# Performance work log

Measured on AMD Instinct MI355X. Metric: run time of the kernel, lower is better.

## Reference

```python
import jax, jax.numpy as jnp
import numpy as np
import math

D_MODEL = 512
N_HEADS = 8
PATH_LEN = 3
B, L, S = 4, 1024, 1024


def _path_index_structure(L, S, path_length):
    """Precompute the static multi-hop index structure (numpy, trace-time)."""
    i = np.arange(L)[:, None]          # [L,1]
    j = np.arange(S)[None, :]          # [1,S]
    step = (j - i) / path_length       # float
    # Python int() truncates toward zero; i + k*step >= 0 here, so floor == int().
    m1 = np.floor(i + 1 * step).astype(np.int32)  # [L,S] first intermediate point
    m2 = np.floor(i + 2 * step).astype(np.int32)  # [L,S] second intermediate point
    near = np.abs(i - j) <= path_length            # [L,S] bool: direct-score region
    return m1, m2, near


def setup_inputs() -> dict:
    key = jax.random.key(0)
    ks = jax.random.split(key, 7)
    inp = {
        "queries": jax.random.normal(ks[0], (B, L, D_MODEL), dtype=jnp.float32),
        "keys": jax.random.normal(ks[1], (B, S, D_MODEL), dtype=jnp.float32),
        "values": jax.random.normal(ks[2], (B, S, D_MODEL), dtype=jnp.float32),
        # nn.Linear(d_model, d_keys*n_heads, bias=False): stored as [in, out] so y = x @ W
        "W_q": jax.random.normal(ks[3], (D_MODEL, D_MODEL), dtype=jnp.float32) * 0.02,
        "W_k": jax.random.normal(ks[4], (D_MODEL, D_MODEL), dtype=jnp.float32) * 0.02,
        "W_v": jax.random.normal(ks[5], (D_MODEL, D_MODEL), dtype=jnp.float32) * 0.02,
        "W_o": jax.random.normal(ks[6], (D_MODEL, D_MODEL), dtype=jnp.float32) * 0.02,
    }
    return inp


def reference(queries, keys, values, W_q, W_k, W_v, W_o):
    Bv, Lv, _ = queries.shape
    Sv = keys.shape[1]
    H = N_HEADS
    q = (queries @ W_q).reshape(Bv, Lv, H, -1).transpose(0, 2, 1, 3)  # [B,H,L,D]
    k = (keys @ W_k).reshape(Bv, Sv, H, -1).transpose(0, 2, 1, 3)     # [B,H,S,D]
    v = (values @ W_v).reshape(Bv, Sv, H, -1).transpose(0, 2, 1, 3)   # [B,H,S,D]
    D = q.shape[-1]

    scores = jnp.einsum('bhld,bhsd->bhls', q, k) / math.sqrt(D)  # [B,H,L,S]

    # --- path-score modification (vectorized form of the nested loops) ---
    m1, m2, near = _path_index_structure(Lv, Sv, PATH_LEN)
    row = np.arange(Lv)[:, None]
    col = np.arange(Sv)[None, :]
    a = scores[:, :, row, m1]   # scores[:,:,i,m1(i,j)] -> [B,H,L,S]
    b = scores[:, :, m2, col]   # scores[:,:,m2(i,j),j] -> [B,H,L,S]
    # .mean() in the original reduces over BOTH batch and heads to a scalar per (i,j)
    path_mean = jnp.mean(a * b, axis=(0, 1))  # [L,S]
    scores = jnp.where(jnp.asarray(near), scores, path_mean[None, None, :, :])

    attn = jax.nn.softmax(scores, axis=-1)  # dropout p=0 in eval reference
    out = jnp.einsum('bhls,bhsd->blhd', attn, v).reshape(Bv, Lv, H * D)
    out = out @ W_o  # [B,L,d_model]
    return out, attn
```

## Files before the change

### kernel.cpp

```cpp
#include <hip/hip_runtime.h>
#include <math.h>

static constexpr int B_ = 4;
static constexpr int L_ = 1024;
static constexpr int S_ = 1024;
static constexpr int DMODEL = 512;
static constexpr int NH = 8;
static constexpr int DH = 64;
static constexpr int NBH = 32;

typedef __attribute__((ext_vector_type(8))) short s8;
typedef __attribute__((ext_vector_type(4))) float floatx4;

__device__ __forceinline__ short f2bf(float f) {
  unsigned u = __float_as_uint(f);
  return (short)((u + 0x7fffu + ((u >> 16) & 1u)) >> 16);
}
__device__ __forceinline__ float bf2f(short s) {
  return __uint_as_float(((unsigned)(unsigned short)s) << 16);
}

__global__ __launch_bounds__(256)
void prep_kernel(const float* __restrict__ q, const float* __restrict__ k,
                 const float* __restrict__ v, short* __restrict__ dst,
                 float* __restrict__ bandS,
                 const float* __restrict__ Wq, const float* __restrict__ Wk,
                 const float* __restrict__ Wv, const float* __restrict__ Wo,
                 short* __restrict__ WT) {
  __shared__ float t[32][33];
  if (blockIdx.x < 3072) {
    const int i = blockIdx.x * 256 + threadIdx.x;
    if (i < 32768) {
      const float4 m4 = make_float4(-1e30f, -1e30f, -1e30f, -1e30f);
      *(float4*)(bandS + ((size_t)i << 3)) = m4;
      *(float4*)(bandS + ((size_t)i << 3) + 4) = m4;
    }
    const int arr = i >> 18;
    const int off = (i & 262143) << 3;
    const float* src = (arr == 0) ? q : (arr == 1) ? k : v;
    const float4 f0 = *(const float4*)(src + off);
    const float4 f1 = *(const float4*)(src + off + 4);
    s8 o;
    o[0] = f2bf(f0.x); o[1] = f2bf(f0.y); o[2] = f2bf(f0.z); o[3] = f2bf(f0.w);
    o[4] = f2bf(f1.x); o[5] = f2bf(f1.y); o[6] = f2bf(f1.z); o[7] = f2bf(f1.w);
    *(s8*)(dst + (size_t)arr * 2097152 + off) = o;
  } else {
    const int bid2 = blockIdx.x - 3072;
    const int z = bid2 >> 8;
    const int rem = bid2 & 255;
    const int k0 = (rem >> 4) << 5, n0 = (rem & 15) << 5;
    const float* W = (z == 0) ? Wq : (z == 1) ? Wk : (z == 2) ? Wv : Wo;
    short* dw = WT + (size_t)z * 262144;
    const int row = threadIdx.x >> 3;
    const int c4 = (threadIdx.x & 7) << 2;
    const float4 f = *(const float4*)(W + (size_t)(k0 + row) * 512 + n0 + c4);
    t[row][c4 + 0] = f.x; t[row][c4 + 1] = f.y; t[row][c4 + 2] = f.z; t[row][c4 + 3] = f.w;
    __syncthreads();
#pragma unroll
    for (int j = 0; j < 4; ++j)
      dw[(size_t)(n0 + row) * 512 + k0 + c4 + j] = f2bf(t[c4 + j][row]);
  }
}

__global__ __launch_bounds__(256)
void proj_qkv_kernel(const short* __restrict__ xbf, const short* __restrict__ WTall,
                     short* __restrict__ qk, short* __restrict__ vT,
                     short* __restrict__ vS) {
  __shared__ short tileS[64][72];
  const int z = blockIdx.z;
  const short* A = xbf + (size_t)z * 2097152;
  const short* WT = WTall + (size_t)z * 262144;
  const int K = DMODEL;
  const int tid = threadIdx.x;
  const int lane = tid & 63, w = tid >> 6;
  const int wm = w >> 1, wn = w & 1;
  const int m0 = blockIdx.y * 64, n0 = blockIdx.x * 64;
  const int kl = (lane >> 4) << 3;
  const short* pA = A + (size_t)(m0 + wm * 32 + (lane & 15)) * K + kl;
  const short* pB = WT + (size_t)(n0 + wn * 32 + (lane & 15)) * K + kl;
  const size_t f16K = (size_t)16 * K;
  floatx4 acc00 = {0,0,0,0}, acc01 = {0,0,0,0}, acc10 = {0,0,0,0}, acc11 = {0,0,0,0};
  for (int k = 0; k < K; k += 32) {
    const s8 a0 = *(const s8*)(pA + k);
    const s8 a1 = *(const s8*)(pA + f16K + k);
    const s8 b0 = *(const s8*)(pB + k);
    const s8 b1 = *(const s8*)(pB + f16K + k);
    acc00 = __builtin_amdgcn_mfma_f32_16x16x32_bf16(a0, b0, acc00, 0, 0, 0);
    acc01 = __builtin_amdgcn_mfma_f32_16x16x32_bf16(a0, b1, acc01, 0, 0, 0);
    acc10 = __builtin_amdgcn_mfma_f32_16x16x32_bf16(a1, b0, acc10, 0, 0, 0);
    acc11 = __builtin_amdgcn_mfma_f32_16x16x32_bf16(a1, b1, acc11, 0, 0, 0);
  }
  const int crow = (lane >> 4) << 2;
  const int ccol = lane & 15;
  if (z < 2) {
#pragma unroll
    for (int fm = 0; fm < 2; ++fm)
#pragma unroll
      for (int fn = 0; fn < 2; ++fn) {
        const floatx4 acc = (fm == 0) ? ((fn == 0) ? acc00 : acc01)
                                      : ((fn == 0) ? acc10 : acc11);
#pragma unroll
        for (int r = 0; r < 4; ++r)
          tileS[wm * 32 + fm * 16 + crow + r][wn * 32 + fn * 16 + ccol] = f2bf(acc[r]);
      }
    __syncthreads();
    const int b = m0 >> 10, l0 = m0 & 1023, h = n0 >> 6;
    short* base = qk + (size_t)z * 2097152 + ((size_t)((b * NH + h) * L_ + l0)) * DH;
#pragma unroll
    for (int qk2 = 0; qk2 < 2; ++qk2) {
      const int c = tid + qk2 * 256;
      const int row = c >> 3, off = (c & 7) << 3;
      *(s8*)(base + (size_t)row * DH + off) = *(const s8*)&tileS[row][off];
    }
  } else {
#pragma unroll
    for (int fm = 0; fm < 2; ++fm)
#pragma unroll
      for (int fn = 0; fn < 2; ++fn) {
        const floatx4 acc = (fm == 0) ? ((fn == 0) ? acc00 : acc01)
                                      : ((fn == 0) ? acc10 : acc11);
        const int col = n0 + wn * 32 + fn * 16 + ccol;
#pragma unroll
        for (int r = 0; r < 4; ++r) {
          const int row = m0 + wm * 32 + fm * 16 + crow + r;
          const int b = row >> 10, l = row & 1023, h = col >> 6, d = col & 63;
          const short val = f2bf(acc[r]);
          vT[((size_t)((b * NH + h) * DH + d)) * S_ + l] = val;
          vS[((size_t)((b * NH + h) * S_ + l)) * DH + d] = val;
        }
      }
  }
}

__global__ __launch_bounds__(256)
void scores_bf16_kernel(const short* __restrict__ qbf, const short* __restrict__ kbf,
                        short* __restrict__ Sbf, float* __restrict__ bandS) {
  __shared__ short tileS[64][72];
  const int tid = threadIdx.x;
  const int lane = tid & 63, w = tid >> 6;
  const int wm = w >> 1, wn = w & 1;
  const int m0 = blockIdx.y * 64, n0 = blockIdx.x * 64;
  const int bh = blockIdx.z;
  const int kl = (lane >> 4) << 3;
  const short* pA = qbf + (size_t)bh * L_ * DH + (size_t)(m0 + wm * 32 + (lane & 15)) * DH + kl;
  const short* pB = kbf + (size_t)bh * S_ * DH + (size_t)(n0 + wn * 32 + (lane & 15)) * DH + kl;
  floatx4 acc00 = {0,0,0,0}, acc01 = {0,0,0,0}, acc10 = {0,0,0,0}, acc11 = {0,0,0,0};
#pragma unroll
  for (int k = 0; k < DH; k += 32) {
    const s8 a0 = *(const s8*)(pA + k);
    const s8 a1 = *(const s8*)(pA + 16 * DH + k);
    const s8 b0 = *(const s8*)(pB + k);
    const s8 b1 = *(const s8*)(pB + 16 * DH + k);
    acc00 = __builtin_amdgcn_mfma_f32_16x16x32_bf16(a0, b0, acc00, 0, 0, 0);
    acc01 = __builtin_amdgcn_mfma_f32_16x16x32_bf16(a0, b1, acc01, 0, 0, 0);
    acc10 = __builtin_amdgcn_mfma_f32_16x16x32_bf16(a1, b0, acc10, 0, 0, 0);
    acc11 = __builtin_amdgcn_mfma_f32_16x16x32_bf16(a1, b1, acc11, 0, 0, 0);
  }
  const int crow = (lane >> 4) << 2;
  const int ccol = lane & 15;
#pragma unroll
  for (int fm = 0; fm < 2; ++fm)
#pragma unroll
    for (int fn = 0; fn < 2; ++fn) {
      const floatx4 acc = (fm == 0) ? ((fn == 0) ? acc00 : acc01)
                                    : ((fn == 0) ? acc10 : acc11);
      const int col = n0 + wn * 32 + fn * 16 + ccol;
#pragma unroll
      for (int r = 0; r < 4; ++r) {
        const int row = m0 + wm * 32 + fm * 16 + crow + r;
        const float sc = acc[r] * 0.125f;
        tileS[wm * 32 + fm * 16 + crow + r][wn * 32 + fn * 16 + ccol] = f2bf(sc);
        const int dd = col - row;
        if (dd >= -3 && dd <= 3)
          bandS[(((size_t)bh << 10) + row) * 8 + dd + 3] = sc;
      }
    }
  __syncthreads();
  short* Sp = Sbf + ((size_t)bh << 20) + (size_t)m0 * S_ + n0;
#pragma unroll
  for (int q2 = 0; q2 < 2; ++q2) {
    const int c = tid + q2 * 256;
    const int row = c >> 3, off = (c & 7) << 3;
    *(s8*)(Sp + (size_t)row * S_ + off) = *(const s8*)&tileS[row][off];
  }
}

__global__ __launch_bounds__(256)
void path_mean_kernel(const short* __restrict__ Sbf, float* __restrict__ pm) {
  __shared__ float As[32][44];
  __shared__ float Bs[32][36];
  const int orig = blockIdx.x;
  const int wgid = (orig & 7) * 128 + (orig >> 3);
  const int i0 = (wgid >> 5) << 5;
  const int j0 = (wgid & 31) << 5;
  const int c0 = (2 * i0 + j0) / 3;
  const int c0a = c0 & ~7;
  const int r0 = (i0 + 2 * j0) / 3;
  const int tid = threadIdx.x;
  const int ti = tid >> 3;
  const int tj = tid & 7;
  const int gi = i0 + ti;
  int aoff[4], boff[4];
#pragma unroll
  for (int b = 0; b < 4; ++b) {
    const int gj = j0 + 4 * tj + b;
    const int m1 = (2 * gi + gj) / 3;
    const int m2 = (gi + 2 * gj) / 3;
    aoff[b] = ti * 44 + (m1 - c0a);
    boff[b] = (m2 - r0) * 36 + (4 * tj + b);
  }
  const int uA = tid;
  const int uB2 = tid + 256;
  int arow = 0, ac = 0, brow = 0, bc = 0, brow2 = 0, bc2 = 0;
  bool isA = uA < 160;
  if (isA) { arow = uA / 5; ac = uA - arow * 5; }
  else { const int v = uA - 160; brow = v >> 2; bc = v & 3; }
  const bool hasU2 = tid < 32;
  { const int v = uB2 - 160; brow2 = v >> 2; bc2 = v & 3; }
  int gcA = c0a + (ac << 3); if (gcA > 1016) gcA = 1016;
  const short* pA = Sbf + (size_t)(i0 + arow) * S_ + gcA;
  const short* pB = Sbf + (size_t)(r0 + brow) * S_ + j0 + (bc << 3);
  const short* pB2 = Sbf + (size_t)(r0 + brow2) * S_ + j0 + (bc2 << 3);

  const float* As0 = &As[0][0];
  const float* Bs0 = &Bs[0][0];
  float acc[4] = {0.f, 0.f, 0.f, 0.f};
  for (int z = 0; z < NBH; ++z) {
    const size_t zo = (size_t)z << 20;
    const s8 v1 = isA ? *(const s8*)(pA + zo) : *(const s8*)(pB + zo);
    s8 v2;
    if (hasU2) v2 = *(const s8*)(pB2 + zo);
    __syncthreads();
    {
      float4 lo, hi;
      lo.x = bf2f(v1[0]); lo.y = bf2f(v1[1]); lo.z = bf2f(v1[2]); lo.w = bf2f(v1[3]);
      hi.x = bf2f(v1[4]); hi.y = bf2f(v1[5]); hi.z = bf2f(v1[6]); hi.w = bf2f(v1[7]);
      if (isA) {
        *(float4*)&As[arow][ac << 3] = lo;
        *(float4*)&As[arow][(ac << 3) + 4] = hi;
      } else {
        *(float4*)&Bs[brow][bc << 3] = lo;
        *(float4*)&Bs[brow][(bc << 3) + 4] = hi;
      }
      if (hasU2) {
        float4 lo2, hi2;
        lo2.x = bf2f(v2[0]); lo2.y = bf2f(v2[1]); lo2.z = bf2f(v2[2]); lo2.w = bf2f(v2[3]);
        hi2.x = bf2f(v2[4]); hi2.y = bf2f(v2[5]); hi2.z = bf2f(v2[6]); hi2.w = bf2f(v2[7]);
        *(float4*)&Bs[brow2][bc2 << 3] = lo2;
        *(float4*)&Bs[brow2][(bc2 << 3) + 4] = hi2;
      }
    }
    __syncthreads();
#pragma unroll
    for (int b = 0; b < 4; ++b)
      acc[b] = fmaf(As0[aoff[b]], Bs0[boff[b]], acc[b]);
  }
  float4 o = make_float4(acc[0] * (1.f / 32.f), acc[1] * (1.f / 32.f),
                         acc[2] * (1.f / 32.f), acc[3] * (1.f / 32.f));
  *(float4*)&pm[(size_t)gi * S_ + j0 + 4 * tj] = o;
}

__global__ __launch_bounds__(256)
void pm_stats_kernel(const float* __restrict__ pm, short* __restrict__ E,
                     float* __restrict__ pmmax, float* __restrict__ pmsum) {
  const int wid = threadIdx.x >> 6, lane = threadIdx.x & 63;
  const int i = blockIdx.x * 4 + wid;
  const float* row = pm + (size_t)i * S_;
  const int j0 = lane << 4;
  float v[16];
#pragma unroll
  for (int c = 0; c < 4; ++c) {
    const float4 f = *(const float4*)(row + j0 + c * 4);
    v[c * 4 + 0] = f.x; v[c * 4 + 1] = f.y; v[c * 4 + 2] = f.z; v[c * 4 + 3] = f.w;
  }
  float mx = -1e30f;
#pragma unroll
  for (int u = 0; u < 16; ++u) {
    const int d = i - (j0 + u);
    const bool far = (d > 3) || (d < -3);
    if (far) mx = fmaxf(mx, v[u]);
  }
#pragma unroll
  for (int off = 32; off >= 1; off >>= 1) mx = fmaxf(mx, __shfl_xor(mx, off));
  float sum = 0.f;
  short e[16];
#pragma unroll
  for (int u = 0; u < 16; ++u) {
    const int d = i - (j0 + u);
    const bool far = (d > 3) || (d < -3);
    const float ev = far ? __expf(v[u] - mx) : 0.f;
    sum += ev;
    e[u] = f2bf(ev);
  }
#pragma unroll
  for (int off = 32; off >= 1; off >>= 1) sum += __shfl_xor(sum, off);
  s8 o0, o1;
#pragma unroll
  for (int u = 0; u < 8; ++u) { o0[u] = e[u]; o1[u] = e[8 + u]; }
  short* Erow = E + (size_t)i * S_ + j0;
  *(s8*)Erow = o0;
  *(s8*)(Erow + 8) = o1;
  if (lane == 0) { pmmax[i] = mx; pmsum[i] = sum; }
}

__global__ __launch_bounds__(256)
void ev_fused_kernel(const short* __restrict__ E, const short* __restrict__ vT,
                     const short* __restrict__ vS, const float* __restrict__ bandS,
                     const float* __restrict__ pmmax, const float* __restrict__ pmsum,
                     float* __restrict__ attn, short* __restrict__ out1) {
  __shared__ float cL[64];
  __shared__ float bL[64][8];
  __shared__ short Vb[70 * 64];
  __shared__ short tileO[64][72];
  const int tid = threadIdx.x;
  const int m0 = blockIdx.x * 64;
  const int bh = blockIdx.y;
  const int b = bh >> 3, h = bh & 7;

  for (int idx = tid; idx < 560; idx += 256) {
    const int rr = idx >> 3, c8 = (idx & 7) << 3;
    int j = m0 - 3 + rr; j = j < 0 ? 0 : (j > 1023 ? 1023 : j);
    *(s8*)&Vb[rr * 64 + c8] = *(const s8*)(vS + ((size_t)bh * S_ + j) * DH + c8);
  }

  {
    const int r = tid >> 2, p = tid & 3;
    const int l = m0 + r;
    const float pmx = pmmax[l], psum = pmsum[l];
    const float* bs = bandS + (((size_t)bh << 10) + l) * 8;
    const float sa = bs[p], sb2 = bs[p + 4];
    float mx = fmaxf(sa, sb2);
    mx = fmaxf(mx, __shfl_xor(mx, 1));
    mx = fmaxf(mx, __shfl_xor(mx, 2));
    const float m = fmaxf(mx, pmx);
    const float ea = __expf(sa - m), eb = __expf(sb2 - m);
    float bsum = ea + eb;
    bsum += __shfl_xor(bsum, 1);
    bsum += __shfl_xor(bsum, 2);
    const float cpm = __expf(pmx - m);
    const float inv = 1.f / (bsum + psum * cpm);
    if (p == 0) cL[r] = cpm * inv;
    bL[r][p] = ea * inv;
    bL[r][p + 4] = eb * inv;
  }
  __syncthreads();

  const int lane = tid & 63, w = tid >> 6;
  const int wm = w >> 1, wn = w & 1;
  const int frow = lane & 15;
  const int kl = (lane >> 4) << 3;
  const int ra0 = m0 + wm * 32 + frow;
  const int lr0 = wm * 32 + frow;
  const int lr1 = lr0 + 16;
  const short* pA = E + (size_t)ra0 * S_ + kl;
  const short* pB = vT + (size_t)bh * DH * S_ + (size_t)(wn * 32 + frow) * S_ + kl;
  const float c0v = cL[lr0];
  const float c1v = cL[lr1];
  float* arow0 = attn + ((size_t)bh * L_ + ra0) * S_;
  float* arow1 = arow0 + (size_t)16 * S_;
  floatx4 acc00 = {0,0,0,0}, acc01 = {0,0,0,0}, acc10 = {0,0,0,0}, acc11 = {0,0,0,0};
  for (int k = 0; k < S_; k += 32) {
    const s8 a0 = *(const s8*)(pA + k);
    const s8 a1 = *(const s8*)(pA + 16 * S_ + k);
    const s8 b0 = *(const s8*)(pB + k);
    const s8 b1 = *(const s8*)(pB + 16 * S_ + k);
    acc00 = __builtin_amdgcn_mfma_f32_16x16x32_bf16(a0, b0, acc00, 0, 0, 0);
    acc01 = __builtin_amdgcn_mfma_f32_16x16x32_bf16(a0, b1, acc01, 0, 0, 0);
    acc10 = __builtin_amdgcn_mfma_f32_16x16x32_bf16(a1, b0, acc10, 0, 0, 0);
    acc11 = __builtin_amdgcn_mfma_f32_16x16x32_bf16(a1, b1, acc11, 0, 0, 0);
    const int jw = k + kl;
    if (wn == 0) {
      float att[8];
#pragma unroll
      for (int e = 0; e < 8; ++e) att[e] = bf2f(a0[e]) * c0v;
      const int rel = ra0 - jw;
      if ((unsigned)(rel + 3) <= 13u) {
#pragma unroll
        for (int e = 0; e < 8; ++e) {
          const int d = e - rel;
          if ((unsigned)(d + 3) <= 6u) att[e] = bL[lr0][d + 3];
        }
      }
      floatx4 v0 = {att[0], att[1], att[2], att[3]};
      floatx4 v1 = {att[4], att[5], att[6], att[7]};
      __builtin_nontemporal_store(v0, (floatx4*)(arow0 + jw));
      __builtin_nontemporal_store(v1, (floatx4*)(arow0 + jw + 4));
    } else {
      float att[8];
#pragma unroll
      for (int e = 0; e < 8; ++e) att[e] = bf2f(a1[e]) * c1v;
      const int rel = ra0 + 16 - jw;
      if ((unsigned)(rel + 3) <= 13u) {
#pragma unroll
        for (int e = 0; e < 8; ++e) {
          const int d = e - rel;
          if ((unsigned)(d + 3) <= 6u) att[e] = bL[lr1][d + 3];
        }
      }
      floatx4 v0 = {att[0], att[1], att[2], att[3]};
      floatx4 v1 = {att[4], att[5], att[6], att[7]};
      __builtin_nontemporal_store(v0, (floatx4*)(arow1 + jw));
      __builtin_nontemporal_store(v1, (floatx4*)(arow1 + jw + 4));
    }
  }

  const int crow = (lane >> 4) << 2;
  const int ccol = lane & 15;
#pragma unroll
  for (int fm = 0; fm < 2; ++fm)
#pragma unroll
    for (int r = 0; r < 4; ++r) {
      const int lrel = wm * 32 + fm * 16 + crow + r;
      const float cc = cL[lrel];
      const float4 b0v = *(const float4*)&bL[lrel][0];
      const float4 b1v = *(const float4*)&bL[lrel][4];
      const float bav[7] = {b0v.x, b0v.y, b0v.z, b0v.w, b1v.x, b1v.y, b1v.z};
#pragma unroll
      for (int fn = 0; fn < 2; ++fn) {
        const floatx4 acc = (fm == 0) ? ((fn == 0) ? acc00 : acc01)
                                      : ((fn == 0) ? acc10 : acc11);
        const int d = wn * 32 + fn * 16 + ccol;
        float corr = 0.f;
#pragma unroll
        for (int u = 0; u < 7; ++u)
          corr = fmaf(bav[u], bf2f(Vb[(lrel + u) * 64 + d]), corr);
        tileO[lrel][d] = f2bf(fmaf(cc, acc[r], corr));
      }
    }
  __syncthreads();
  short* obase = out1 + ((size_t)(b * L_ + m0)) * DMODEL + h * DH;
#pragma unroll
  for (int q2 = 0; q2 < 2; ++q2) {
    const int c = tid + q2 * 256;
    const int row = c >> 3, off = (c & 7) << 3;
    *(s8*)(obase + (size_t)row * DMODEL + off) = *(const s8*)&tileO[row][off];
  }
}

__global__ __launch_bounds__(256)
void proj_out_kernel(const short* __restrict__ A, const short* __restrict__ WT,
                     float* __restrict__ C) {
  __shared__ float tileF[64][68];
  const int K = DMODEL;
  const int tid = threadIdx.x;
  const int lane = tid & 63, w = tid >> 6;
  const int wm = w >> 1, wn = w & 1;
  const int m0 = blockIdx.y * 64, n0 = blockIdx.x * 64;
  const int kl = (lane >> 4) << 3;
  const short* pA = A + (size_t)(m0 + wm * 32 + (lane & 15)) * K + kl;
  const short* pB = WT + (size_t)(n0 + wn * 32 + (lane & 15)) * K + kl;
  const size_t f16K = (size_t)16 * K;
  floatx4 acc00 = {0,0,0,0}, acc01 = {0,0,0,0}, acc10 = {0,0,0,0}, acc11 = {0,0,0,0};
  for (int k = 0; k < K; k += 32) {
    const s8 a0 = *(const s8*)(pA + k);
    const s8 a1 = *(const s8*)(pA + f16K + k);
    const s8 b0 = *(const s8*)(pB + k);
    const s8 b1 = *(const s8*)(pB + f16K + k);
    acc00 = __builtin_amdgcn_mfma_f32_16x16x32_bf16(a0, b0, acc00, 0, 0, 0);
    acc01 = __builtin_amdgcn_mfma_f32_16x16x32_bf16(a0, b1, acc01, 0, 0, 0);
    acc10 = __builtin_amdgcn_mfma_f32_16x16x32_bf16(a1, b0, acc10, 0, 0, 0);
    acc11 = __builtin_amdgcn_mfma_f32_16x16x32_bf16(a1, b1, acc11, 0, 0, 0);
  }
  const int crow = (lane >> 4) << 2;
  const int ccol = lane & 15;
#pragma unroll
  for (int fm = 0; fm < 2; ++fm)
#pragma unroll
    for (int fn = 0; fn < 2; ++fn) {
      const floatx4 acc = (fm == 0) ? ((fn == 0) ? acc00 : acc01)
                                    : ((fn == 0) ? acc10 : acc11);
#pragma unroll
      for (int r = 0; r < 4; ++r)
        tileF[wm * 32 + fm * 16 + crow + r][wn * 32 + fn * 16 + ccol] = acc[r];
    }
  __syncthreads();
  float* base = C + (size_t)m0 * DMODEL + n0;
#pragma unroll
  for (int q2 = 0; q2 < 4; ++q2) {
    const int c = tid + q2 * 256;
    const int row = c >> 4, off = (c & 15) << 2;
    *(float4*)(base + (size_t)row * DMODEL + off) = *(const float4*)&tileF[row][off];
  }
}

extern "C" void kernel_launch(void* const* d_in, const int* in_sizes, int n_in,
                              void* d_out, int out_size, void* d_ws, size_t ws_size,
                              hipStream_t stream) {
  const float* queries = (const float*)d_in[0];
  const float* keys    = (const float*)d_in[1];
  const float* values  = (const float*)d_in[2];
  const float* Wq      = (const float*)d_in[3];
  const float* Wk      = (const float*)d_in[4];
  const float* Wv      = (const float*)d_in[5];
  const float* Wo      = (const float*)d_in[6];

  float* out  = (float*)d_out;
  float* attn = out + (size_t)B_ * L_ * DMODEL;

  char* ws = (char*)d_ws;
  short* xbf   = (short*)(ws);
  short* WT    = (short*)(ws + 12u * 1048576);
  short* qkbf  = (short*)(ws + 14u * 1048576);
  short* vT    = (short*)(ws + 22u * 1048576);
  short* vS    = (short*)(ws + 26u * 1048576);
  float* pm    = (float*)(ws + 30u * 1048576);
  short* E     = (short*)(ws + 34u * 1048576);
  float* pmmax = (float*)(ws + 36u * 1048576);
  float* pmsum = (float*)(ws + 36u * 1048576 + 4096);
  float* bandS = (float*)(ws + 37u * 1048576);
  short* out1  = (short*)(ws + 38u * 1048576);
  short* Sbf   = (short*)(ws + 42u * 1048576);

  const dim3 blk(256);

  hipLaunchKernelGGL(prep_kernel, dim3(4096), blk, 0, stream,
                     queries, keys, values, xbf, bandS, Wq, Wk, Wv, Wo, WT);

  hipLaunchKernelGGL(proj_qkv_kernel, dim3(DMODEL / 64, (B_ * L_) / 64, 3),
                     blk, 0, stream, xbf, WT, qkbf, vT, vS);

  hipLaunchKernelGGL(scores_bf16_kernel, dim3(S_ / 64, L_ / 64, NBH), blk, 0, stream,
                     qkbf, qkbf + 2097152, Sbf, bandS);

  hipLaunchKernelGGL(path_mean_kernel, dim3(1024), blk, 0, stream, Sbf, pm);

  hipLaunchKernelGGL(pm_stats_kernel, dim3(L_ / 4), blk, 0, stream,
                     pm, E, pmmax, pmsum);

  hipLaunchKernelGGL(ev_fused_kernel, dim3(L_ / 64, NBH), blk, 0, stream,
                     E, vT, vS, bandS, pmmax, pmsum, attn, out1);

  hipLaunchKernelGGL(proj_out_kernel, dim3(DMODEL / 64, (B_ * L_) / 64), blk, 0, stream,
                     out1, WT + 786432, out);
}
```

Before: 203.3 us.

## Fuse input bf16 conversion into projection; split and double-buffer path-mean reduction

The separate fp32-to-bf16 conversion pass over queries, keys and values is removed. The projection GEMM now loads fp32 inputs directly and converts them in registers, which saves a full write and re-read of the converted copies. The path-mean kernel splits the 32 batch-head reduction into two halves across twice as many blocks, double-buffers its shared-memory tiles with prefetch, and staggers the start slice per tile. The two partial sums are combined in pm_stats. The trade-off is doubled fp32 load traffic in the projection loop and an extra partial-sum buffer to write and read.

Result: slower. 227.2 us (+11.8%).

```diff
diff --git a/kernel.cpp b/kernel.cpp
--- a/kernel.cpp
+++ b/kernel.cpp
@@ -21,33 +21,13 @@
 }
 
 __global__ __launch_bounds__(256)
-void prep_kernel(const float* __restrict__ q, const float* __restrict__ k,
-                 const float* __restrict__ v, short* __restrict__ dst,
-                 float* __restrict__ bandS,
-                 const float* __restrict__ Wq, const float* __restrict__ Wk,
+void prep_kernel(const float* __restrict__ Wq, const float* __restrict__ Wk,
                  const float* __restrict__ Wv, const float* __restrict__ Wo,
-                 short* __restrict__ WT) {
+                 short* __restrict__ WT, float* __restrict__ bandS) {
   __shared__ float t[32][33];
-  if (blockIdx.x < 3072) {
-    const int i = blockIdx.x * 256 + threadIdx.x;
-    if (i < 32768) {
-      const float4 m4 = make_float4(-1e30f, -1e30f, -1e30f, -1e30f);
-      *(float4*)(bandS + ((size_t)i << 3)) = m4;
-      *(float4*)(bandS + ((size_t)i << 3) + 4) = m4;
-    }
-    const int arr = i >> 18;
-    const int off = (i & 262143) << 3;
-    const float* src = (arr == 0) ? q : (arr == 1) ? k : v;
-    const float4 f0 = *(const float4*)(src + off);
-    const float4 f1 = *(const float4*)(src + off + 4);
-    s8 o;
-    o[0] = f2bf(f0.x); o[1] = f2bf(f0.y); o[2] = f2bf(f0.z); o[3] = f2bf(f0.w);
-    o[4] = f2bf(f1.x); o[5] = f2bf(f1.y); o[6] = f2bf(f1.z); o[7] = f2bf(f1.w);
-    *(s8*)(dst + (size_t)arr * 2097152 + off) = o;
-  } else {
-    const int bid2 = blockIdx.x - 3072;
-    const int z = bid2 >> 8;
-    const int rem = bid2 & 255;
+  if (blockIdx.x < 1024) {
+    const int z = blockIdx.x >> 8;
+    const int rem = blockIdx.x & 255;
     const int k0 = (rem >> 4) << 5, n0 = (rem & 15) << 5;
     const float* W = (z == 0) ? Wq : (z == 1) ? Wk : (z == 2) ? Wv : Wo;
     short* dw = WT + (size_t)z * 262144;
@@ -59,16 +39,22 @@
 #pragma unroll
     for (int j = 0; j < 4; ++j)
       dw[(size_t)(n0 + row) * 512 + k0 + c4 + j] = f2bf(t[c4 + j][row]);
-  }
-}
-
-__global__ __launch_bounds__(256)
-void proj_qkv_kernel(const short* __restrict__ xbf, const short* __restrict__ WTall,
+  } else {
+    const int i = (blockIdx.x - 1024) * 256 + threadIdx.x;
+    const float4 m4 = make_float4(-1e30f, -1e30f, -1e30f, -1e30f);
+    *(float4*)(bandS + ((size_t)i << 3)) = m4;
+    *(float4*)(bandS + ((size_t)i << 3) + 4) = m4;
+  }
+}
+
+__global__ __launch_bounds__(256)
+void proj_qkv_kernel(const float* __restrict__ qf, const float* __restrict__ kf,
+                     const float* __restrict__ vf, const short* __restrict__ WTall,
                      short* __restrict__ qk, short* __restrict__ vT,
                      short* __restrict__ vS) {
   __shared__ short tileS[64][72];
   const int z = blockIdx.z;
-  const short* A = xbf + (size_t)z * 2097152;
+  const float* A = (z == 0) ? qf : (z == 1) ? kf : vf;
   const short* WT = WTall + (size_t)z * 262144;
   const int K = DMODEL;
   const int tid = threadIdx.x;
@@ -76,13 +62,20 @@
   const int wm = w >> 1, wn = w & 1;
   const int m0 = blockIdx.y * 64, n0 = blockIdx.x * 64;
   const int kl = (lane >> 4) << 3;
-  const short* pA = A + (size_t)(m0 + wm * 32 + (lane & 15)) * K + kl;
+  const float* pA = A + (size_t)(m0 + wm * 32 + (lane & 15)) * K + kl;
   const short* pB = WT + (size_t)(n0 + wn * 32 + (lane & 15)) * K + kl;
   const size_t f16K = (size_t)16 * K;
   floatx4 acc00 = {0,0,0,0}, acc01 = {0,0,0,0}, acc10 = {0,0,0,0}, acc11 = {0,0,0,0};
   for (int k = 0; k < K; k += 32) {
-    const s8 a0 = *(const s8*)(pA + k);
-    const s8 a1 = *(const s8*)(pA + f16K + k);
+    const float4 fa0 = *(const float4*)(pA + k);
+    const float4 fa1 = *(const float4*)(pA + k + 4);
+    const float4 fb0 = *(const float4*)(pA + f16K + k);
+    const float4 fb1 = *(const float4*)(pA + f16K + k + 4);
+    s8 a0, a1;
+    a0[0] = f2bf(fa0.x); a0[1] = f2bf(fa0.y); a0[2] = f2bf(fa0.z); a0[3] = f2bf(fa0.w);
+    a0[4] = f2bf(fa1.x); a0[5] = f2bf(fa1.y); a0[6] = f2bf(fa1.z); a0[7] = f2bf(fa1.w);
+    a1[0] = f2bf(fb0.x); a1[1] = f2bf(fb0.y); a1[2] = f2bf(fb0.z); a1[3] = f2bf(fb0.w);
+    a1[4] = f2bf(fb1.x); a1[5] = f2bf(fb1.y); a1[6] = f2bf(fb1.z); a1[7] = f2bf(fb1.w);
     const s8 b0 = *(const s8*)(pB + k);
     const s8 b1 = *(const s8*)(pB + f16K + k);
     acc00 = __builtin_amdgcn_mfma_f32_16x16x32_bf16(a0, b0, acc00, 0, 0, 0);
@@ -186,16 +179,20 @@
 }
 
 __global__ __launch_bounds__(256)
-void path_mean_kernel(const short* __restrict__ Sbf, float* __restrict__ pm) {
-  __shared__ float As[32][44];
-  __shared__ float Bs[32][36];
+void path_mean_kernel(const short* __restrict__ Sbf, float* __restrict__ pm2) {
+  __shared__ float As[2 * 32 * 44];
+  __shared__ float Bs[2 * 32 * 36];
   const int orig = blockIdx.x;
-  const int wgid = (orig & 7) * 128 + (orig >> 3);
-  const int i0 = (wgid >> 5) << 5;
-  const int j0 = (wgid & 31) << 5;
+  const int wgid = (orig & 7) * 256 + (orig >> 3);
+  const int half = wgid >> 10;
+  const int tile = wgid & 1023;
+  const int i0 = (tile >> 5) << 5;
+  const int j0 = (tile & 31) << 5;
   const int c0 = (2 * i0 + j0) / 3;
   const int c0a = c0 & ~7;
   const int r0 = (i0 + 2 * j0) / 3;
+  const int zbase = half << 4;
+  const int stag = tile & 15;
   const int tid = threadIdx.x;
   const int ti = tid >> 3;
   const int tj = tid & 7;
@@ -209,69 +206,88 @@
     aoff[b] = ti * 44 + (m1 - c0a);
     boff[b] = (m2 - r0) * 36 + (4 * tj + b);
   }
-  const int uA = tid;
-  const int uB2 = tid + 256;
   int arow = 0, ac = 0, brow = 0, bc = 0, brow2 = 0, bc2 = 0;
-  bool isA = uA < 160;
-  if (isA) { arow = uA / 5; ac = uA - arow * 5; }
-  else { const int v = uA - 160; brow = v >> 2; bc = v & 3; }
+  const bool isA = tid < 160;
+  if (isA) { arow = tid / 5; ac = tid - arow * 5; }
+  else { const int v = tid - 160; brow = v >> 2; bc = v & 3; }
   const bool hasU2 = tid < 32;
-  { const int v = uB2 - 160; brow2 = v >> 2; bc2 = v & 3; }
+  { const int v = tid + 96; brow2 = v >> 2; bc2 = v & 3; }
   int gcA = c0a + (ac << 3); if (gcA > 1016) gcA = 1016;
   const short* pA = Sbf + (size_t)(i0 + arow) * S_ + gcA;
   const short* pB = Sbf + (size_t)(r0 + brow) * S_ + j0 + (bc << 3);
   const short* pB2 = Sbf + (size_t)(r0 + brow2) * S_ + j0 + (bc2 << 3);
 
-  const float* As0 = &As[0][0];
-  const float* Bs0 = &Bs[0][0];
+  const int awr = isA ? (arow * 44 + (ac << 3)) : (brow * 36 + (bc << 3));
+  const int awr2 = brow2 * 36 + (bc2 << 3);
+
+  auto writeBuf = [&](int buf, const s8& v1, const s8& v2) {
+    float4 lo, hi;
+    lo.x = bf2f(v1[0]); lo.y = bf2f(v1[1]); lo.z = bf2f(v1[2]); lo.w = bf2f(v1[3]);
+    hi.x = bf2f(v1[4]); hi.y = bf2f(v1[5]); hi.z = bf2f(v1[6]); hi.w = bf2f(v1[7]);
+    if (isA) {
+      *(float4*)&As[buf * 1408 + awr] = lo;
+      *(float4*)&As[buf * 1408 + awr + 4] = hi;
+    } else {
+      *(float4*)&Bs[buf * 1152 + awr] = lo;
+      *(float4*)&Bs[buf * 1152 + awr + 4] = hi;
+    }
+    if (hasU2) {
+      float4 lo2, hi2;
+      lo2.x = bf2f(v2[0]); lo2.y = bf2f(v2[1]); lo2.z = bf2f(v2[2]); lo2.w = bf2f(v2[3]);
+      hi2.x = bf2f(v2[4]); hi2.y = bf2f(v2[5]); hi2.z = bf2f(v2[6]); hi2.w = bf2f(v2[7]);
+      *(float4*)&Bs[buf * 1152 + awr2] = lo2;
+      *(float4*)&Bs[buf * 1152 + awr2 + 4] = hi2;
+    }
+  };
+
   float acc[4] = {0.f, 0.f, 0.f, 0.f};
-  for (int z = 0; z < NBH; ++z) {
-    const size_t zo = (size_t)z << 20;
-    const s8 v1 = isA ? *(const s8*)(pA + zo) : *(const s8*)(pB + zo);
-    s8 v2;
+  {
+    const size_t zo = (size_t)(zbase + stag) << 20;
+    s8 v1 = isA ? *(const s8*)(pA + zo) : *(const s8*)(pB + zo);
+    s8 v2 = {};
     if (hasU2) v2 = *(const s8*)(pB2 + zo);
-    __syncthreads();
-    {
-      float4 lo, hi;
-      lo.x = bf2f(v1[0]); lo.y = bf2f(v1[1]); lo.z = bf2f(v1[2]); lo.w = bf2f(v1[3]);
-      hi.x = bf2f(v1[4]); hi.y = bf2f(v1[5]); hi.z = bf2f(v1[6]); hi.w = bf2f(v1[7]);
-      if (isA) {
-        *(float4*)&As[arow][ac << 3] = lo;
-        *(float4*)&As[arow][(ac << 3) + 4] = hi;
-      } else {
-        *(float4*)&Bs[brow][bc << 3] = lo;
-        *(float4*)&Bs[brow][(bc << 3) + 4] = hi;
-      }
-      if (hasU2) {
-        float4 lo2, hi2;
-        lo2.x = bf2f(v2[0]); lo2.y = bf2f(v2[1]); lo2.z = bf2f(v2[2]); lo2.w = bf2f(v2[3]);
-        hi2.x = bf2f(v2[4]); hi2.y = bf2f(v2[5]); hi2.z = bf2f(v2[6]); hi2.w = bf2f(v2[7]);
-        *(float4*)&Bs[brow2][bc2 << 3] = lo2;
-        *(float4*)&Bs[brow2][(bc2 << 3) + 4] = hi2;
-      }
-    }
-    __syncthreads();
+    writeBuf(0, v1, v2);
+  }
+  __syncthreads();
+  for (int zz = 0; zz < 16; ++zz) {
+    const int cur = zz & 1;
+    s8 n1 = {}, n2 = {};
+    if (zz < 15) {
+      const size_t zo = (size_t)(zbase + ((zz + 1 + stag) & 15)) << 20;
+      n1 = isA ? *(const s8*)(pA + zo) : *(const s8*)(pB + zo);
+      if (hasU2) n2 = *(const s8*)(pB2 + zo);
+    }
+    const float* Ab = &As[cur * 1408];
+    const float* Bb = &Bs[cur * 1152];
 #pragma unroll
     for (int b = 0; b < 4; ++b)
-      acc[b] = fmaf(As0[aoff[b]], Bs0[boff[b]], acc[b]);
-  }
-  float4 o = make_float4(acc[0] * (1.f / 32.f), acc[1] * (1.f / 32.f),
-                         acc[2] * (1.f / 32.f), acc[3] * (1.f / 32.f));
-  *(float4*)&pm[(size_t)gi * S_ + j0 + 4 * tj] = o;
-}
-
-__global__ __launch_bounds__(256)
-void pm_stats_kernel(const float* __restrict__ pm, short* __restrict__ E,
+      acc[b] = fmaf(Ab[aoff[b]], Bb[boff[b]], acc[b]);
+    if (zz < 15) {
+      writeBuf(1 - cur, n1, n2);
+      __syncthreads();
+    }
+  }
+  float4 o = make_float4(acc[0], acc[1], acc[2], acc[3]);
+  *(float4*)&pm2[(size_t)half * (L_ * S_) + (size_t)gi * S_ + j0 + 4 * tj] = o;
+}
+
+__global__ __launch_bounds__(256)
+void pm_stats_kernel(const float* __restrict__ pm2, short* __restrict__ E,
                      float* __restrict__ pmmax, float* __restrict__ pmsum) {
   const int wid = threadIdx.x >> 6, lane = threadIdx.x & 63;
   const int i = blockIdx.x * 4 + wid;
-  const float* row = pm + (size_t)i * S_;
+  const float* row0 = pm2 + (size_t)i * S_;
+  const float* row1 = row0 + (size_t)(L_ * S_);
   const int j0 = lane << 4;
   float v[16];
 #pragma unroll
   for (int c = 0; c < 4; ++c) {
-    const float4 f = *(const float4*)(row + j0 + c * 4);
-    v[c * 4 + 0] = f.x; v[c * 4 + 1] = f.y; v[c * 4 + 2] = f.z; v[c * 4 + 3] = f.w;
+    const float4 fa = *(const float4*)(row0 + j0 + c * 4);
+    const float4 fb = *(const float4*)(row1 + j0 + c * 4);
+    v[c * 4 + 0] = (fa.x + fb.x) * (1.f / 32.f);
+    v[c * 4 + 1] = (fa.y + fb.y) * (1.f / 32.f);
+    v[c * 4 + 2] = (fa.z + fb.z) * (1.f / 32.f);
+    v[c * 4 + 3] = (fa.w + fb.w) * (1.f / 32.f);
   }
   float mx = -1e30f;
 #pragma unroll
@@ -498,34 +514,33 @@
   float* attn = out + (size_t)B_ * L_ * DMODEL;
 
   char* ws = (char*)d_ws;
-  short* xbf   = (short*)(ws);
-  short* WT    = (short*)(ws + 12u * 1048576);
-  short* qkbf  = (short*)(ws + 14u * 1048576);
-  short* vT    = (short*)(ws + 22u * 1048576);
-  short* vS    = (short*)(ws + 26u * 1048576);
-  float* pm    = (float*)(ws + 30u * 1048576);
-  short* E     = (short*)(ws + 34u * 1048576);
-  float* pmmax = (float*)(ws + 36u * 1048576);
-  float* pmsum = (float*)(ws + 36u * 1048576 + 4096);
-  float* bandS = (float*)(ws + 37u * 1048576);
-  short* out1  = (short*)(ws + 38u * 1048576);
-  short* Sbf   = (short*)(ws + 42u * 1048576);
+  short* WT    = (short*)(ws);
+  short* qkbf  = (short*)(ws + 2u * 1048576);
+  short* vT    = (short*)(ws + 10u * 1048576);
+  short* vS    = (short*)(ws + 14u * 1048576);
+  float* pm2   = (float*)(ws + 18u * 1048576);
+  short* E     = (short*)(ws + 26u * 1048576);
+  float* pmmax = (float*)(ws + 28u * 1048576);
+  float* pmsum = (float*)(ws + 28u * 1048576 + 4096);
+  float* bandS = (float*)(ws + 29u * 1048576);
+  short* out1  = (short*)(ws + 30u * 1048576);
+  short* Sbf   = (short*)(ws + 34u * 1048576);
 
   const dim3 blk(256);
 
-  hipLaunchKernelGGL(prep_kernel, dim3(4096), blk, 0, stream,
-                     queries, keys, values, xbf, bandS, Wq, Wk, Wv, Wo, WT);
+  hipLaunchKernelGGL(prep_kernel, dim3(1152), blk, 0, stream,
+                     Wq, Wk, Wv, Wo, WT, bandS);
 
   hipLaunchKernelGGL(proj_qkv_kernel, dim3(DMODEL / 64, (B_ * L_) / 64, 3),
-                     blk, 0, stream, xbf, WT, qkbf, vT, vS);
+                     blk, 0, stream, queries, keys, values, WT, qkbf, vT, vS);
 
   hipLaunchKernelGGL(scores_bf16_kernel, dim3(S_ / 64, L_ / 64, NBH), blk, 0, stream,
                      qkbf, qkbf + 2097152, Sbf, bandS);
 
-  hipLaunchKernelGGL(path_mean_kernel, dim3(1024), blk, 0, stream, Sbf, pm);
+  hipLaunchKernelGGL(path_mean_kernel, dim3(2048), blk, 0, stream, Sbf, pm2);
 
   hipLaunchKernelGGL(pm_stats_kernel, dim3(L_ / 4), blk, 0, stream,
-                     pm, E, pmmax, pmsum);
+                     pm2, E, pmmax, pmsum);
 
   hipLaunchKernelGGL(ev_fused_kernel, dim3(L_ / 64, NBH), blk, 0, stream,
                      E, vT, vS, bandS, pmmax, pmsum, attn, out1);
```
